# Optimization experiments

Hardware: AMD Instinct MI355X
Metric: run time of the kernel (lower is better)

Reference implementation:

```python
import jax, jax.numpy as jnp
import numpy as np

BN_EPS = 1e-5


def _gru(x, Wih, Whh, bih, bhh):
    # x: [B,S,D]; Wih: [3H,D]; Whh: [3H,H]; PyTorch gate order (r, z, n)
    B, S, D = x.shape
    H = Whh.shape[1]
    xg = jnp.einsum('bsd,gd->bsg', x, Wih) + bih  # [B,S,3H] precomputed input gates

    def step(h, xg_t):
        hg = h @ Whh.T + bhh
        xr, xz, xn = jnp.split(xg_t, 3, axis=-1)
        hr, hz, hn = jnp.split(hg, 3, axis=-1)
        r = jax.nn.sigmoid(xr + hr)
        z = jax.nn.sigmoid(xz + hz)
        n = jnp.tanh(xn + r * hn)
        h_new = (1.0 - z) * n + z * h
        return h_new, h_new

    h0 = jnp.zeros((B, H), x.dtype)
    _, hs = jax.lax.scan(step, h0, jnp.swapaxes(xg, 0, 1))  # [S,B,H]
    return jnp.swapaxes(hs, 0, 1)


def _lstm(x, Wih, Whh, bih, bhh):
    # x: [B,S,D]; PyTorch gate order (i, f, g, o)
    B, S, D = x.shape
    H = Whh.shape[1]
    xg = jnp.einsum('bsd,gd->bsg', x, Wih) + bih  # [B,S,4H]

    def step(carry, xg_t):
        h, c = carry
        g = xg_t + h @ Whh.T + bhh
        i, f, gg, o = jnp.split(g, 4, axis=-1)
        i = jax.nn.sigmoid(i)
        f = jax.nn.sigmoid(f)
        gg = jnp.tanh(gg)
        o = jax.nn.sigmoid(o)
        c_new = f * c + i * gg
        h_new = o * jnp.tanh(c_new)
        return (h_new, c_new), h_new

    h0 = jnp.zeros((B, H), x.dtype)
    c0 = jnp.zeros((B, H), x.dtype)
    _, hs = jax.lax.scan(step, (h0, c0), jnp.swapaxes(xg, 0, 1))
    return jnp.swapaxes(hs, 0, 1)


def setup_inputs() -> dict:
    key = jax.random.key(0)
    B, S, D, H = 64, 512, 40, 512
    ks = jax.random.split(key, 16)
    s_in = 1.0 / np.sqrt(H)

    def u(k, shape):
        return jax.random.uniform(k, shape, jnp.float32, -s_in, s_in)

    inp = {
        'x': jax.random.normal(ks[0], (B, S, D), jnp.float32),
        # rec1: GRU
        'gru_Wih': u(ks[1], (3 * H, D)),
        'gru_Whh': u(ks[2], (3 * H, H)),
        'gru_bih': u(ks[3], (3 * H,)),
        'gru_bhh': u(ks[4], (3 * H,)),
        # rec2: LSTM over [x, ssr] -> input D+1
        'lstm_Wih': u(ks[5], (4 * H, D + 1)),
        'lstm_Whh': u(ks[6], (4 * H, H)),
        'lstm_bih': u(ks[7], (4 * H,)),
        'lstm_bhh': u(ks[8], (4 * H,)),
        # fc1/fc2/fc3: hidden -> 1
        'fc1_w': u(ks[9], (1, H)), 'fc1_b': u(ks[10], (1,)),
        'fc2_w': u(ks[11], (1, H)), 'fc2_b': u(ks[12], (1,)),
        'fc3_w': u(ks[13], (1, H)), 'fc3_b': u(ks[14], (1,)),
        # BatchNorm1d affine params
        'bn_gamma': jnp.ones((H,), jnp.float32),
        'bn_beta': jnp.zeros((H,), jnp.float32),
    }
    return inp


def reference(x, gru_Wih, gru_Whh, gru_bih, gru_bhh,
              lstm_Wih, lstm_Whh, lstm_bih, lstm_bhh,
              fc1_w, fc1_b, fc2_w, fc2_b, fc3_w, fc3_b,
              bn_gamma, bn_beta):
    B, S, D = x.shape
    o1 = _gru(x, gru_Wih, gru_Whh, gru_bih, gru_bhh)  # [B,S,H]
    # BatchNorm1d (training mode): per-channel stats over (batch, time)
    mean = jnp.mean(o1, axis=(0, 1))
    var = jnp.mean((o1 - mean) ** 2, axis=(0, 1))
    o1 = (o1 - mean) * jax.lax.rsqrt(var + BN_EPS) * bn_gamma + bn_beta
    # gated scalar channel (dropout p=0 is identity)
    sr = jax.nn.relu(o1 @ fc1_w.T + fc1_b)            # [B,S,1]
    w = jnp.abs(jax.nn.sigmoid(o1 @ fc2_w.T + fc2_b))  # [B,S,1]
    ssr = sr * (w + 1.0)                              # [B,S,1]
    x2 = jnp.concatenate([x, ssr], axis=2)            # [B,S,D+1]
    o2 = _lstm(x2, lstm_Wih, lstm_Whh, lstm_bih, lstm_bhh)
    out = jax.nn.relu(o2 @ fc3_w.T + fc3_b)           # [B,S,1]
    return out, ssr
```

## Files before the change

kernel.cpp:

```cpp
#include <hip/hip_runtime.h>
#include <stdint.h>

#define MB 16
#define GW 16
#define NU 32
#define HD 512
#define SEQ 512
#define DX 40

using short8 = __attribute__((ext_vector_type(8))) short;
using f32x4  = __attribute__((ext_vector_type(4))) float;

__device__ __forceinline__ unsigned short f2bf(float f) {
  uint32_t u = __builtin_bit_cast(uint32_t, f);
  u += 0x7fffu + ((u >> 16) & 1u);
  return (unsigned short)(u >> 16);
}
__device__ __forceinline__ float sigm(float x) { return 1.0f / (1.0f + __expf(-x)); }


__global__ __launch_bounds__(512, 2) void gru_kernel(
    const float* __restrict__ x, const float* __restrict__ Wih,
    const float* __restrict__ Whh, const float* __restrict__ bih,
    const float* __restrict__ bhh, unsigned* __restrict__ flags,
    unsigned short* __restrict__ hbuf, float* __restrict__ o1,
    float* __restrict__ stats)
{
  const int wg = blockIdx.x & (GW - 1);
  const int g  = blockIdx.x >> 4;
  const int tid = threadIdx.x;
  const int wave = tid >> 6;
  const int lane = tid & 63;
  const int u0 = wg * NU;
  const int bg = g * MB;

  __shared__ unsigned short h_s[MB][520];
  __shared__ unsigned short x_s[MB][72];
  __shared__ float gate_s[3][MB][NU];
  __shared__ float xn_s[MB][NU];

  for (int i = tid; i < MB * 32; i += 512) x_s[i >> 5][40 + (i & 31)] = 0;

  short8 bfrag[18];
  const int myGate = wave >> 1;
  const int ut = wave & 1;
  const int kq = (lane >> 4) * 8;
  if (wave < 6) {
    const int row = myGate * HD + u0 + ut * 16 + (lane & 15);
    for (int kt = 0; kt < 16; ++kt) {
      const float* p = Whh + (size_t)row * HD + kt * 32 + kq;
      short8 f;
#pragma unroll
      for (int j = 0; j < 8; ++j) f[j] = (short)f2bf(p[j]);
      bfrag[kt] = f;
    }
    for (int kt = 16; kt < 18; ++kt) {
      short8 f;
#pragma unroll
      for (int j = 0; j < 8; ++j) {
        int c = kt * 32 + kq + j - HD;
        float v = (myGate < 2 && c < DX) ? Wih[(size_t)row * DX + c] : 0.0f;
        f[j] = (short)f2bf(v);
      }
      bfrag[kt] = f;
    }
  } else {
    const int row = 2 * HD + u0 + (wave - 6) * 16 + (lane & 15);
    for (int kt = 0; kt < 2; ++kt) {
      short8 f;
#pragma unroll
      for (int j = 0; j < 8; ++j) {
        int c = kt * 32 + kq + j;
        f[j] = (short)((c < DX) ? f2bf(Wih[(size_t)row * DX + c]) : 0);
      }
      bfrag[kt] = f;
    }
  }

  const int sb = tid >> 5;
  const int su = tid & 31;
  float hprev = 0.0f, ssum = 0.0f, ssq = 0.0f;
  const float b_r  = bih[u0 + su] + bhh[u0 + su];
  const float b_z  = bih[HD + u0 + su] + bhh[HD + u0 + su];
  const float b_in = bih[2 * HD + u0 + su];
  const float b_hn = bhh[2 * HD + u0 + su];

  unsigned* gf = flags + g * GW * 16;
  unsigned* myProdFlag = gf + ((tid & 127) >> 3) * 16;

  for (int t = 0; t < SEQ; ++t) {
    const unsigned long long* hin64 =
        (const unsigned long long*)(hbuf + ((size_t)g * 2 + (t & 1)) * MB * HD);
    uint32_t* hout32 =
        (uint32_t*)(hbuf + ((size_t)g * 2 + ((t + 1) & 1)) * MB * HD);

    {
      while (__hip_atomic_load(myProdFlag, __ATOMIC_RELAXED,
                               __HIP_MEMORY_SCOPE_AGENT) < (unsigned)t)
        __builtin_amdgcn_s_sleep(1);
#pragma unroll
      for (int it = 0; it < 4; ++it) {
        int q = it * 512 + tid;
        unsigned long long v = __hip_atomic_load(hin64 + q, __ATOMIC_RELAXED,
                                                 __HIP_MEMORY_SCOPE_AGENT);
        *(unsigned long long*)(&h_s[q >> 7][(q & 127) * 4]) = v;
      }
    }
    {
      int b = tid >> 5, c = tid & 31;
      const float* xr = x + ((size_t)(bg + b) * SEQ + t) * DX;
      x_s[b][c] = f2bf(xr[c]);
      if (c < 8) x_s[b][32 + c] = f2bf(xr[32 + c]);
    }
    __syncthreads();

    if (wave < 6) {
      const int m = lane & 15;
      f32x4 acc = {0.f, 0.f, 0.f, 0.f};
#pragma unroll
      for (int kt = 0; kt < 16; ++kt) {
        short8 a = *(const short8*)(&h_s[m][kt * 32 + kq]);
        acc = __builtin_amdgcn_mfma_f32_16x16x32_bf16(a, bfrag[kt], acc, 0, 0, 0);
      }
      short8 ax0 = *(const short8*)(&x_s[m][kq]);
      short8 ax1 = *(const short8*)(&x_s[m][32 + kq]);
      acc = __builtin_amdgcn_mfma_f32_16x16x32_bf16(ax0, bfrag[16], acc, 0, 0, 0);
      acc = __builtin_amdgcn_mfma_f32_16x16x32_bf16(ax1, bfrag[17], acc, 0, 0, 0);
#pragma unroll
      for (int r = 0; r < 4; ++r)
        gate_s[myGate][(lane >> 4) * 4 + r][ut * 16 + (lane & 15)] = acc[r];
    } else {
      const int m = lane & 15;
      f32x4 acc = {0.f, 0.f, 0.f, 0.f};
      short8 ax0 = *(const short8*)(&x_s[m][kq]);
      short8 ax1 = *(const short8*)(&x_s[m][32 + kq]);
      acc = __builtin_amdgcn_mfma_f32_16x16x32_bf16(ax0, bfrag[0], acc, 0, 0, 0);
      acc = __builtin_amdgcn_mfma_f32_16x16x32_bf16(ax1, bfrag[1], acc, 0, 0, 0);
#pragma unroll
      for (int r = 0; r < 4; ++r)
        xn_s[(lane >> 4) * 4 + r][(wave - 6) * 16 + (lane & 15)] = acc[r];
    }
    __syncthreads();

    float r_ = sigm(gate_s[0][sb][su] + b_r);
    float z_ = sigm(gate_s[1][sb][su] + b_z);
    float n_ = tanhf(xn_s[sb][su] + b_in + r_ * (gate_s[2][sb][su] + b_hn));
    float h = (1.0f - z_) * n_ + z_ * hprev;
    hprev = h;
    ssum += h; ssq += h * h;
    {
      float hp = __shfl_xor(h, 1);
      if ((tid & 1) == 0) {
        uint32_t packed = (uint32_t)f2bf(h) | ((uint32_t)f2bf(hp) << 16);
        __hip_atomic_store(hout32 + ((sb * HD + u0 + su) >> 1), packed,
                           __ATOMIC_RELAXED, __HIP_MEMORY_SCOPE_AGENT);
      }
    }
    __syncthreads();

    if (tid == 0)
      __hip_atomic_store(gf + wg * 16, (unsigned)(t + 1), __ATOMIC_RELAXED,
                         __HIP_MEMORY_SCOPE_AGENT);
    o1[((size_t)(bg + sb) * SEQ + t) * HD + u0 + su] = h;
  }

  atomicAdd(&stats[u0 + su], ssum);
  atomicAdd(&stats[HD + u0 + su], ssq);
}

__global__ __launch_bounds__(512, 2) void lstm_kernel(
    const float* __restrict__ x, const float* __restrict__ Wih,
    const float* __restrict__ Whh, const float* __restrict__ bih,
    const float* __restrict__ bhh, const float* __restrict__ ssr,
    unsigned* __restrict__ flags, unsigned short* __restrict__ hbuf,
    float* __restrict__ o2)
{
  const int wg = blockIdx.x & (GW - 1);
  const int g  = blockIdx.x >> 4;
  const int tid = threadIdx.x;
  const int wave = tid >> 6;
  const int lane = tid & 63;
  const int u0 = wg * NU;
  const int bg = g * MB;

  __shared__ unsigned short h_s[MB][520];
  __shared__ unsigned short x_s[MB][72];
  __shared__ float gate_s[4][MB][NU];

  for (int i = tid; i < MB * 32; i += 512) x_s[i >> 5][40 + (i & 31)] = 0;

  short8 bfrag[18];
  const int myGate = wave >> 1;
  const int ut = wave & 1;
  const int kq = (lane >> 4) * 8;
  {
    const int row = myGate * HD + u0 + ut * 16 + (lane & 15);
    for (int kt = 0; kt < 16; ++kt) {
      const float* p = Whh + (size_t)row * HD + kt * 32 + kq;
      short8 f;
#pragma unroll
      for (int j = 0; j < 8; ++j) f[j] = (short)f2bf(p[j]);
      bfrag[kt] = f;
    }
    for (int kt = 16; kt < 18; ++kt) {
      short8 f;
#pragma unroll
      for (int j = 0; j < 8; ++j) {
        int c = kt * 32 + kq + j - HD;
        float v = (c < 41) ? Wih[(size_t)row * 41 + c] : 0.0f;
        f[j] = (short)f2bf(v);
      }
      bfrag[kt] = f;
    }
  }

  const int sb = tid >> 5;
  const int su = tid & 31;
  float creg = 0.0f;
  const float b_i = bih[u0 + su] + bhh[u0 + su];
  const float b_f = bih[HD + u0 + su] + bhh[HD + u0 + su];
  const float b_g = bih[2 * HD + u0 + su] + bhh[2 * HD + u0 + su];
  const float b_o = bih[3 * HD + u0 + su] + bhh[3 * HD + u0 + su];

  unsigned* gf = flags + g * GW * 16;
  unsigned* myProdFlag = gf + ((tid & 127) >> 3) * 16;

  for (int t = 0; t < SEQ; ++t) {
    const unsigned long long* hin64 =
        (const unsigned long long*)(hbuf + ((size_t)g * 2 + (t & 1)) * MB * HD);
    uint32_t* hout32 =
        (uint32_t*)(hbuf + ((size_t)g * 2 + ((t + 1) & 1)) * MB * HD);

    {
      while (__hip_atomic_load(myProdFlag, __ATOMIC_RELAXED,
                               __HIP_MEMORY_SCOPE_AGENT) < (unsigned)t)
        __builtin_amdgcn_s_sleep(1);
#pragma unroll
      for (int it = 0; it < 4; ++it) {
        int q = it * 512 + tid;
        unsigned long long v = __hip_atomic_load(hin64 + q, __ATOMIC_RELAXED,
                                                 __HIP_MEMORY_SCOPE_AGENT);
        *(unsigned long long*)(&h_s[q >> 7][(q & 127) * 4]) = v;
      }
    }
    {
      int b = tid >> 5, c = tid & 31;
      const float* xr = x + ((size_t)(bg + b) * SEQ + t) * DX;
      x_s[b][c] = f2bf(xr[c]);
      if (c < 8) x_s[b][32 + c] = f2bf(xr[32 + c]);
      if (c == 8) x_s[b][40] = f2bf(ssr[(size_t)(bg + b) * SEQ + t]);
    }
    __syncthreads();

    {
      const int m = lane & 15;
      f32x4 acc = {0.f, 0.f, 0.f, 0.f};
#pragma unroll
      for (int kt = 0; kt < 16; ++kt) {
        short8 a = *(const short8*)(&h_s[m][kt * 32 + kq]);
        acc = __builtin_amdgcn_mfma_f32_16x16x32_bf16(a, bfrag[kt], acc, 0, 0, 0);
      }
      short8 ax0 = *(const short8*)(&x_s[m][kq]);
      short8 ax1 = *(const short8*)(&x_s[m][32 + kq]);
      acc = __builtin_amdgcn_mfma_f32_16x16x32_bf16(ax0, bfrag[16], acc, 0, 0, 0);
      acc = __builtin_amdgcn_mfma_f32_16x16x32_bf16(ax1, bfrag[17], acc, 0, 0, 0);
#pragma unroll
      for (int r = 0; r < 4; ++r)
        gate_s[myGate][(lane >> 4) * 4 + r][ut * 16 + (lane & 15)] = acc[r];
    }
    __syncthreads();

    float gi = sigm(gate_s[0][sb][su] + b_i);
    float gf_ = sigm(gate_s[1][sb][su] + b_f);
    float gg = tanhf(gate_s[2][sb][su] + b_g);
    float go = sigm(gate_s[3][sb][su] + b_o);
    creg = gf_ * creg + gi * gg;
    float h = go * tanhf(creg);
    {
      float hp = __shfl_xor(h, 1);
      if ((tid & 1) == 0) {
        uint32_t packed = (uint32_t)f2bf(h) | ((uint32_t)f2bf(hp) << 16);
        __hip_atomic_store(hout32 + ((sb * HD + u0 + su) >> 1), packed,
                           __ATOMIC_RELAXED, __HIP_MEMORY_SCOPE_AGENT);
      }
    }
    __syncthreads();

    if (tid == 0)
      __hip_atomic_store(gf + wg * 16, (unsigned)(t + 1), __ATOMIC_RELAXED,
                         __HIP_MEMORY_SCOPE_AGENT);
    o2[((size_t)(bg + sb) * SEQ + t) * HD + u0 + su] = h;
  }
}

__global__ __launch_bounds__(512) void coef_kernel(
    const float* __restrict__ stats, const float* __restrict__ fc1_w,
    const float* __restrict__ fc1_b, const float* __restrict__ fc2_w,
    const float* __restrict__ fc2_b, const float* __restrict__ gamma,
    const float* __restrict__ beta, float* __restrict__ coef)
{
  __shared__ float r1[512], r2[512];
  const int j = threadIdx.x;
  const float inv_n = 1.0f / 32768.0f;
  float mean = stats[j] * inv_n;
  float var = stats[HD + j] * inv_n - mean * mean;
  float scale = gamma[j] * rsqrtf(var + 1e-5f);
  float shift = beta[j] - mean * scale;
  coef[j] = fc1_w[j] * scale;
  coef[HD + j] = fc2_w[j] * scale;
  r1[j] = fc1_w[j] * shift;
  r2[j] = fc2_w[j] * shift;
  __syncthreads();
  for (int s = 256; s > 0; s >>= 1) {
    if (j < s) { r1[j] += r1[j + s]; r2[j] += r2[j + s]; }
    __syncthreads();
  }
  if (j == 0) {
    coef[2 * HD] = r1[0] + fc1_b[0];
    coef[2 * HD + 1] = r2[0] + fc2_b[0];
  }
}

__global__ __launch_bounds__(256) void ssr_kernel(
    const float* __restrict__ o1, const float* __restrict__ coef,
    float* __restrict__ ssr_ws, float* __restrict__ dssr)
{
  const int row = blockIdx.x * 4 + (threadIdx.x >> 6);
  const int lane = threadIdx.x & 63;
  const float* p = o1 + (size_t)row * HD + lane * 8;
  float s1 = 0.f, s2 = 0.f;
#pragma unroll
  for (int j = 0; j < 8; ++j) {
    float v = p[j];
    s1 += v * coef[lane * 8 + j];
    s2 += v * coef[HD + lane * 8 + j];
  }
#pragma unroll
  for (int off = 32; off > 0; off >>= 1) {
    s1 += __shfl_down(s1, off);
    s2 += __shfl_down(s2, off);
  }
  if (lane == 0) {
    float sr = fmaxf(s1 + coef[2 * HD], 0.0f);
    float w = fabsf(sigm(s2 + coef[2 * HD + 1]));
    float v = sr * (1.0f + w);
    ssr_ws[row] = v;
    dssr[row] = v;
  }
}

__global__ __launch_bounds__(256) void out_kernel(
    const float* __restrict__ o2, const float* __restrict__ fc3_w,
    const float* __restrict__ fc3_b, float* __restrict__ dout)
{
  const int row = blockIdx.x * 4 + (threadIdx.x >> 6);
  const int lane = threadIdx.x & 63;
  const float* p = o2 + (size_t)row * HD + lane * 8;
  float s = 0.f;
#pragma unroll
  for (int j = 0; j < 8; ++j) s += p[j] * fc3_w[lane * 8 + j];
#pragma unroll
  for (int off = 32; off > 0; off >>= 1) s += __shfl_down(s, off);
  if (lane == 0) dout[row] = fmaxf(s + fc3_b[0], 0.0f);
}

extern "C" void kernel_launch(void* const* d_in, const int* in_sizes, int n_in,
                              void* d_out, int out_size, void* d_ws, size_t ws_size,
                              hipStream_t stream) {
  (void)in_sizes; (void)n_in; (void)out_size; (void)ws_size;
  const float* x    = (const float*)d_in[0];
  const float* gWih = (const float*)d_in[1];
  const float* gWhh = (const float*)d_in[2];
  const float* gbih = (const float*)d_in[3];
  const float* gbhh = (const float*)d_in[4];
  const float* lWih = (const float*)d_in[5];
  const float* lWhh = (const float*)d_in[6];
  const float* lbih = (const float*)d_in[7];
  const float* lbhh = (const float*)d_in[8];
  const float* fc1w = (const float*)d_in[9];
  const float* fc1b = (const float*)d_in[10];
  const float* fc2w = (const float*)d_in[11];
  const float* fc2b = (const float*)d_in[12];
  const float* fc3w = (const float*)d_in[13];
  const float* fc3b = (const float*)d_in[14];
  const float* gam  = (const float*)d_in[15];
  const float* bet  = (const float*)d_in[16];
  float* out = (float*)d_out;

  char* ws = (char*)d_ws;
  unsigned* flags_g = (unsigned*)(ws + 0);
  unsigned* flags_l = (unsigned*)(ws + 4096);
  float* stats      = (float*)(ws + 8192);
  float* coef       = (float*)(ws + 16384);
  float* ssr_ws     = (float*)(ws + 32768);
  unsigned short* hbuf_g = (unsigned short*)(ws + 262144);
  unsigned short* hbuf_l = (unsigned short*)(ws + 393216);
  float* o1 = (float*)(ws + 1048576);
  float* o2 = o1 + (size_t)64 * SEQ * HD;

  hipMemsetAsync(ws, 0, 12288, stream);
  hipMemsetAsync(ws + 262144, 0, 262144, stream);

  gru_kernel<<<dim3(64), dim3(512), 0, stream>>>(x, gWih, gWhh, gbih, gbhh,
                                                 flags_g, hbuf_g, o1, stats);
  coef_kernel<<<dim3(1), dim3(512), 0, stream>>>(stats, fc1w, fc1b, fc2w, fc2b,
                                                 gam, bet, coef);
  ssr_kernel<<<dim3(8192), dim3(256), 0, stream>>>(o1, coef, ssr_ws, out + 32768);
  lstm_kernel<<<dim3(64), dim3(512), 0, stream>>>(x, lWih, lWhh, lbih, lbhh, ssr_ws,
                                                  flags_l, hbuf_l, o2);
  out_kernel<<<dim3(8192), dim3(256), 0, stream>>>(o2, fc3w, fc3b, out);
}
```

Measured before the change: 3.240 ms.

## Warp-specialize recurrent kernels with dedicated communication waves and LDS spin sync

Adds two communication waves per workgroup in both the GRU and LSTM kernels (640 threads). These waves publish the packed hidden state to global memory, raise the cross-block flag, and prefetch the next step's h and x into double-buffered LDS. The compute waves swap __syncthreads for counter-based LDS spin waits, and the elementwise threads now handle two batch rows each. Splitting the MFMA accumulation into two chains shortens the dependency latency. The aim is to take global communication and the full barriers off the per-step critical path, at the cost of more complex synchronisation and possible memory-ordering fragility.

Measured after the change: 3.542 ms. 1.09x slower.

```diff
diff --git a/kernel.cpp b/kernel.cpp
--- a/kernel.cpp
+++ b/kernel.cpp
@@ -1,15 +1,16 @@
 #include <hip/hip_runtime.h>
 #include <stdint.h>
 
-#define MB 16
 #define GW 16
 #define NU 32
 #define HD 512
 #define SEQ 512
 #define DX 40
+#define MB 16
 
 using short8 = __attribute__((ext_vector_type(8))) short;
 using f32x4  = __attribute__((ext_vector_type(4))) float;
+typedef unsigned long long u64;
 
 __device__ __forceinline__ unsigned short f2bf(float f) {
   uint32_t u = __builtin_bit_cast(uint32_t, f);
@@ -18,13 +19,14 @@
 }
 __device__ __forceinline__ float sigm(float x) { return 1.0f / (1.0f + __expf(-x)); }
 
-
-__global__ __launch_bounds__(512, 2) void gru_kernel(
+#define MFMA_B16(a, b, c) __builtin_amdgcn_mfma_f32_16x16x32_bf16((a), (b), (c), 0, 0, 0)
+
+
+__global__ __launch_bounds__(640, 1) void gru_kernel(
     const float* __restrict__ x, const float* __restrict__ Wih,
     const float* __restrict__ Whh, const float* __restrict__ bih,
     const float* __restrict__ bhh, unsigned* __restrict__ flags,
-    unsigned short* __restrict__ hbuf, float* __restrict__ o1,
-    float* __restrict__ stats)
+    u64* __restrict__ hbuf, float* __restrict__ o1, float* __restrict__ stats)
 {
   const int wg = blockIdx.x & (GW - 1);
   const int g  = blockIdx.x >> 4;
@@ -34,12 +36,12 @@
   const int u0 = wg * NU;
   const int bg = g * MB;
 
-  __shared__ unsigned short h_s[MB][520];
-  __shared__ unsigned short x_s[MB][72];
+  __shared__ __align__(16) unsigned short h_s[2][MB][520];
+  __shared__ __align__(16) unsigned short x_s[2][MB][72];
   __shared__ float gate_s[3][MB][NU];
   __shared__ float xn_s[MB][NU];
-
-  for (int i = tid; i < MB * 32; i += 512) x_s[i >> 5][40 + (i & 31)] = 0;
+  __shared__ uint32_t h_stage[256];
+  __shared__ uint32_t sync_s[4];
 
   short8 bfrag[18];
   const int myGate = wave >> 1;
@@ -64,7 +66,7 @@
       }
       bfrag[kt] = f;
     }
-  } else {
+  } else if (wave < 8) {
     const int row = 2 * HD + u0 + (wave - 6) * 16 + (lane & 15);
     for (int kt = 0; kt < 2; ++kt) {
       short8 f;
@@ -79,100 +81,166 @@
 
   const int sb = tid >> 5;
   const int su = tid & 31;
-  float hprev = 0.0f, ssum = 0.0f, ssq = 0.0f;
-  const float b_r  = bih[u0 + su] + bhh[u0 + su];
-  const float b_z  = bih[HD + u0 + su] + bhh[HD + u0 + su];
-  const float b_in = bih[2 * HD + u0 + su];
-  const float b_hn = bhh[2 * HD + u0 + su];
+  float b_r = 0.f, b_z = 0.f, b_in = 0.f, b_hn = 0.f;
+  if (tid < 256) {
+    b_r  = bih[u0 + su] + bhh[u0 + su];
+    b_z  = bih[HD + u0 + su] + bhh[HD + u0 + su];
+    b_in = bih[2 * HD + u0 + su];
+    b_hn = bhh[2 * HD + u0 + su];
+  }
+
+  for (int i = tid; i < 4160; i += 640) ((u64*)h_s)[i] = 0ull;
+  for (int i = tid; i < 576;  i += 640) ((u64*)x_s)[i] = 0ull;
+  if (tid < 4) sync_s[tid] = 0;
+  __syncthreads();
+  {
+    int r = tid / 40, c = tid % 40;
+    x_s[0][r][c] = f2bf(x[((size_t)(bg + r) * SEQ) * DX + c]);
+  }
+  __syncthreads();
 
   unsigned* gf = flags + g * GW * 16;
-  unsigned* myProdFlag = gf + ((tid & 127) >> 3) * 16;
-
-  for (int t = 0; t < SEQ; ++t) {
-    const unsigned long long* hin64 =
-        (const unsigned long long*)(hbuf + ((size_t)g * 2 + (t & 1)) * MB * HD);
-    uint32_t* hout32 =
-        (uint32_t*)(hbuf + ((size_t)g * 2 + ((t + 1) & 1)) * MB * HD);
-
-    {
-      while (__hip_atomic_load(myProdFlag, __ATOMIC_RELAXED,
-                               __HIP_MEMORY_SCOPE_AGENT) < (unsigned)t)
+
+  if (wave < 8) {
+    float hpA = 0.f, hpB = 0.f, ssum = 0.f, ssq = 0.f;
+    for (int t = 0; t < SEQ; ++t) {
+      if (t) {
+        while (__hip_atomic_load(&sync_s[2], __ATOMIC_ACQUIRE,
+                                 __HIP_MEMORY_SCOPE_WORKGROUP) < 2u * (unsigned)t)
+          __builtin_amdgcn_s_sleep(1);
+      }
+      const int p = t & 1;
+      if (wave < 6) {
+        const int m = lane & 15;
+        f32x4 a0 = {0.f, 0.f, 0.f, 0.f}, a1 = {0.f, 0.f, 0.f, 0.f};
+#pragma unroll
+        for (int kt = 0; kt < 16; kt += 2) {
+          short8 ha0 = *(const short8*)(&h_s[p][m][kt * 32 + kq]);
+          short8 ha1 = *(const short8*)(&h_s[p][m][(kt + 1) * 32 + kq]);
+          a0 = MFMA_B16(ha0, bfrag[kt], a0);
+          a1 = MFMA_B16(ha1, bfrag[kt + 1], a1);
+        }
+        short8 ax0 = *(const short8*)(&x_s[p][m][kq]);
+        short8 ax1 = *(const short8*)(&x_s[p][m][32 + kq]);
+        a0 = MFMA_B16(ax0, bfrag[16], a0);
+        a1 = MFMA_B16(ax1, bfrag[17], a1);
+        f32x4 acc = a0 + a1;
+#pragma unroll
+        for (int r = 0; r < 4; ++r)
+          gate_s[myGate][(lane >> 4) * 4 + r][ut * 16 + (lane & 15)] = acc[r];
+      } else {
+        const int m = lane & 15;
+        f32x4 acc = {0.f, 0.f, 0.f, 0.f};
+        short8 ax0 = *(const short8*)(&x_s[p][m][kq]);
+        short8 ax1 = *(const short8*)(&x_s[p][m][32 + kq]);
+        acc = MFMA_B16(ax0, bfrag[0], acc);
+        acc = MFMA_B16(ax1, bfrag[1], acc);
+#pragma unroll
+        for (int r = 0; r < 4; ++r)
+          xn_s[(lane >> 4) * 4 + r][(wave - 6) * 16 + (lane & 15)] = acc[r];
+      }
+      asm volatile("s_waitcnt lgkmcnt(0)" ::: "memory");
+      if (lane == 0)
+        __hip_atomic_fetch_add(&sync_s[0], 1u, __ATOMIC_RELAXED,
+                               __HIP_MEMORY_SCOPE_WORKGROUP);
+      if (tid < 256) {
+        while (__hip_atomic_load(&sync_s[0], __ATOMIC_ACQUIRE,
+                                 __HIP_MEMORY_SCOPE_WORKGROUP) < 8u * (unsigned)(t + 1))
+          __builtin_amdgcn_s_sleep(1);
+        float rA = sigm(gate_s[0][sb][su] + b_r);
+        float zA = sigm(gate_s[1][sb][su] + b_z);
+        float nA = tanhf(xn_s[sb][su] + b_in + rA * (gate_s[2][sb][su] + b_hn));
+        float hA = (1.0f - zA) * nA + zA * hpA;
+        float rB = sigm(gate_s[0][sb + 8][su] + b_r);
+        float zB = sigm(gate_s[1][sb + 8][su] + b_z);
+        float nB = tanhf(xn_s[sb + 8][su] + b_in + rB * (gate_s[2][sb + 8][su] + b_hn));
+        float hB = (1.0f - zB) * nB + zB * hpB;
+        hpA = hA; hpB = hB;
+        ssum += hA + hB; ssq += hA * hA + hB * hB;
+        o1[((size_t)(bg + sb) * SEQ + t) * HD + u0 + su] = hA;
+        o1[((size_t)(bg + sb + 8) * SEQ + t) * HD + u0 + su] = hB;
+        float pA = __shfl_xor(hA, 1);
+        float pB = __shfl_xor(hB, 1);
+        if ((su & 1) == 0) {
+          h_stage[sb * 16 + (su >> 1)] =
+              (uint32_t)f2bf(hA) | ((uint32_t)f2bf(pA) << 16);
+          h_stage[(sb + 8) * 16 + (su >> 1)] =
+              (uint32_t)f2bf(hB) | ((uint32_t)f2bf(pB) << 16);
+        }
+        asm volatile("s_waitcnt lgkmcnt(0)" ::: "memory");
+        if (lane == 0)
+          __hip_atomic_fetch_add(&sync_s[1], 1u, __ATOMIC_RELAXED,
+                                 __HIP_MEMORY_SCOPE_WORKGROUP);
+      }
+    }
+    if (tid < 256) {
+      atomicAdd(&stats[u0 + su], ssum);
+      atomicAdd(&stats[HD + u0 + su], ssq);
+    }
+  } else {
+    const int ct = tid - 512;
+    const int prow = ct >> 3;
+    const int pquad = ct & 7;
+    unsigned* myFlag = gf + prow * 16;
+    for (int u = 0; u < SEQ - 1; ++u) {
+      while (__hip_atomic_load(&sync_s[1], __ATOMIC_ACQUIRE,
+                               __HIP_MEMORY_SCOPE_WORKGROUP) < 4u * (unsigned)(u + 1))
         __builtin_amdgcn_s_sleep(1);
-#pragma unroll
-      for (int it = 0; it < 4; ++it) {
-        int q = it * 512 + tid;
-        unsigned long long v = __hip_atomic_load(hin64 + q, __ATOMIC_RELAXED,
-                                                 __HIP_MEMORY_SCOPE_AGENT);
-        *(unsigned long long*)(&h_s[q >> 7][(q & 127) * 4]) = v;
-      }
-    }
-    {
-      int b = tid >> 5, c = tid & 31;
-      const float* xr = x + ((size_t)(bg + b) * SEQ + t) * DX;
-      x_s[b][c] = f2bf(xr[c]);
-      if (c < 8) x_s[b][32 + c] = f2bf(xr[32 + c]);
-    }
-    __syncthreads();
-
-    if (wave < 6) {
-      const int m = lane & 15;
-      f32x4 acc = {0.f, 0.f, 0.f, 0.f};
-#pragma unroll
-      for (int kt = 0; kt < 16; ++kt) {
-        short8 a = *(const short8*)(&h_s[m][kt * 32 + kq]);
-        acc = __builtin_amdgcn_mfma_f32_16x16x32_bf16(a, bfrag[kt], acc, 0, 0, 0);
-      }
-      short8 ax0 = *(const short8*)(&x_s[m][kq]);
-      short8 ax1 = *(const short8*)(&x_s[m][32 + kq]);
-      acc = __builtin_amdgcn_mfma_f32_16x16x32_bf16(ax0, bfrag[16], acc, 0, 0, 0);
-      acc = __builtin_amdgcn_mfma_f32_16x16x32_bf16(ax1, bfrag[17], acc, 0, 0, 0);
-#pragma unroll
-      for (int r = 0; r < 4; ++r)
-        gate_s[myGate][(lane >> 4) * 4 + r][ut * 16 + (lane & 15)] = acc[r];
-    } else {
-      const int m = lane & 15;
-      f32x4 acc = {0.f, 0.f, 0.f, 0.f};
-      short8 ax0 = *(const short8*)(&x_s[m][kq]);
-      short8 ax1 = *(const short8*)(&x_s[m][32 + kq]);
-      acc = __builtin_amdgcn_mfma_f32_16x16x32_bf16(ax0, bfrag[0], acc, 0, 0, 0);
-      acc = __builtin_amdgcn_mfma_f32_16x16x32_bf16(ax1, bfrag[1], acc, 0, 0, 0);
-#pragma unroll
-      for (int r = 0; r < 4; ++r)
-        xn_s[(lane >> 4) * 4 + r][(wave - 6) * 16 + (lane & 15)] = acc[r];
-    }
-    __syncthreads();
-
-    float r_ = sigm(gate_s[0][sb][su] + b_r);
-    float z_ = sigm(gate_s[1][sb][su] + b_z);
-    float n_ = tanhf(xn_s[sb][su] + b_in + r_ * (gate_s[2][sb][su] + b_hn));
-    float h = (1.0f - z_) * n_ + z_ * hprev;
-    hprev = h;
-    ssum += h; ssq += h * h;
-    {
-      float hp = __shfl_xor(h, 1);
-      if ((tid & 1) == 0) {
-        uint32_t packed = (uint32_t)f2bf(h) | ((uint32_t)f2bf(hp) << 16);
-        __hip_atomic_store(hout32 + ((sb * HD + u0 + su) >> 1), packed,
-                           __ATOMIC_RELAXED, __HIP_MEMORY_SCOPE_AGENT);
-      }
-    }
-    __syncthreads();
-
-    if (tid == 0)
-      __hip_atomic_store(gf + wg * 16, (unsigned)(t + 1), __ATOMIC_RELAXED,
-                         __HIP_MEMORY_SCOPE_AGENT);
-    o1[((size_t)(bg + sb) * SEQ + t) * HD + u0 + su] = h;
-  }
-
-  atomicAdd(&stats[u0 + su], ssum);
-  atomicAdd(&stats[HD + u0 + su], ssq);
-}
-
-__global__ __launch_bounds__(512, 2) void lstm_kernel(
+      uint32_t w0 = h_stage[prow * 16 + pquad * 2];
+      uint32_t w1 = h_stage[prow * 16 + pquad * 2 + 1];
+      u64 pub = ((u64)w1 << 32) | (u64)w0;
+      u64* hb = hbuf + ((size_t)g * 2 + ((u + 1) & 1)) * 2048;
+      __hip_atomic_store(hb + prow * 128 + wg * 8 + pquad, pub,
+                         __ATOMIC_RELAXED, __HIP_MEMORY_SCOPE_AGENT);
+      asm volatile("s_waitcnt vmcnt(0)" ::: "memory");
+      if (lane == 0)
+        __hip_atomic_fetch_add(&sync_s[3], 1u, __ATOMIC_RELAXED,
+                               __HIP_MEMORY_SCOPE_WORKGROUP);
+      if (wave == 8) {
+        while (__hip_atomic_load(&sync_s[3], __ATOMIC_ACQUIRE,
+                                 __HIP_MEMORY_SCOPE_WORKGROUP) < 2u * (unsigned)(u + 1))
+          __builtin_amdgcn_s_sleep(1);
+        if (lane == 0)
+          __hip_atomic_store(gf + wg * 16, (unsigned)(u + 1),
+                             __ATOMIC_RELAXED, __HIP_MEMORY_SCOPE_AGENT);
+      }
+      float xv[5];
+      const int xi = ct * 5;
+#pragma unroll
+      for (int i = 0; i < 5; ++i) {
+        int idx = xi + i, r = idx / 40, c = idx % 40;
+        xv[i] = x[((size_t)(bg + r) * SEQ + (u + 1)) * DX + c];
+      }
+      while (__hip_atomic_load(myFlag, __ATOMIC_RELAXED,
+                               __HIP_MEMORY_SCOPE_AGENT) < (unsigned)(u + 1))
+        __builtin_amdgcn_s_sleep(1);
+      u64 hv[16];
+#pragma unroll
+      for (int i = 0; i < 16; ++i)
+        hv[i] = __hip_atomic_load(hb + i * 128 + ct, __ATOMIC_RELAXED,
+                                  __HIP_MEMORY_SCOPE_AGENT);
+      const int np = (u + 1) & 1;
+#pragma unroll
+      for (int i = 0; i < 16; ++i)
+        *(u64*)(&h_s[np][i][ct * 4]) = hv[i];
+#pragma unroll
+      for (int i = 0; i < 5; ++i) {
+        int idx = xi + i, r = idx / 40, c = idx % 40;
+        x_s[np][r][c] = f2bf(xv[i]);
+      }
+      asm volatile("s_waitcnt lgkmcnt(0)" ::: "memory");
+      if (lane == 0)
+        __hip_atomic_fetch_add(&sync_s[2], 1u, __ATOMIC_RELAXED,
+                               __HIP_MEMORY_SCOPE_WORKGROUP);
+    }
+  }
+}
+
+__global__ __launch_bounds__(640, 1) void lstm_kernel(
     const float* __restrict__ x, const float* __restrict__ Wih,
     const float* __restrict__ Whh, const float* __restrict__ bih,
     const float* __restrict__ bhh, const float* __restrict__ ssr,
-    unsigned* __restrict__ flags, unsigned short* __restrict__ hbuf,
+    unsigned* __restrict__ flags, u64* __restrict__ hbuf,
     float* __restrict__ o2)
 {
   const int wg = blockIdx.x & (GW - 1);
@@ -183,17 +251,17 @@
   const int u0 = wg * NU;
   const int bg = g * MB;
 
-  __shared__ unsigned short h_s[MB][520];
-  __shared__ unsigned short x_s[MB][72];
+  __shared__ __align__(16) unsigned short h_s[2][MB][520];
+  __shared__ __align__(16) unsigned short x_s[2][MB][72];
   __shared__ float gate_s[4][MB][NU];
-
-  for (int i = tid; i < MB * 32; i += 512) x_s[i >> 5][40 + (i & 31)] = 0;
+  __shared__ uint32_t h_stage[256];
+  __shared__ uint32_t sync_s[4];
 
   short8 bfrag[18];
   const int myGate = wave >> 1;
   const int ut = wave & 1;
   const int kq = (lane >> 4) * 8;
-  {
+  if (wave < 8) {
     const int row = myGate * HD + u0 + ut * 16 + (lane & 15);
     for (int kt = 0; kt < 16; ++kt) {
       const float* p = Whh + (size_t)row * HD + kt * 32 + kq;
@@ -216,80 +284,150 @@
 
   const int sb = tid >> 5;
   const int su = tid & 31;
-  float creg = 0.0f;
-  const float b_i = bih[u0 + su] + bhh[u0 + su];
-  const float b_f = bih[HD + u0 + su] + bhh[HD + u0 + su];
-  const float b_g = bih[2 * HD + u0 + su] + bhh[2 * HD + u0 + su];
-  const float b_o = bih[3 * HD + u0 + su] + bhh[3 * HD + u0 + su];
+  float b_i = 0.f, b_f = 0.f, b_g = 0.f, b_o = 0.f;
+  if (tid < 256) {
+    b_i = bih[u0 + su] + bhh[u0 + su];
+    b_f = bih[HD + u0 + su] + bhh[HD + u0 + su];
+    b_g = bih[2 * HD + u0 + su] + bhh[2 * HD + u0 + su];
+    b_o = bih[3 * HD + u0 + su] + bhh[3 * HD + u0 + su];
+  }
+
+  for (int i = tid; i < 4160; i += 640) ((u64*)h_s)[i] = 0ull;
+  for (int i = tid; i < 576;  i += 640) ((u64*)x_s)[i] = 0ull;
+  if (tid < 4) sync_s[tid] = 0;
+  __syncthreads();
+  {
+    int r = tid / 40, c = tid % 40;
+    x_s[0][r][c] = f2bf(x[((size_t)(bg + r) * SEQ) * DX + c]);
+  }
+  if (tid < 16) x_s[0][tid][40] = f2bf(ssr[(size_t)(bg + tid) * SEQ]);
+  __syncthreads();
 
   unsigned* gf = flags + g * GW * 16;
-  unsigned* myProdFlag = gf + ((tid & 127) >> 3) * 16;
-
-  for (int t = 0; t < SEQ; ++t) {
-    const unsigned long long* hin64 =
-        (const unsigned long long*)(hbuf + ((size_t)g * 2 + (t & 1)) * MB * HD);
-    uint32_t* hout32 =
-        (uint32_t*)(hbuf + ((size_t)g * 2 + ((t + 1) & 1)) * MB * HD);
-
-    {
-      while (__hip_atomic_load(myProdFlag, __ATOMIC_RELAXED,
-                               __HIP_MEMORY_SCOPE_AGENT) < (unsigned)t)
+
+  if (wave < 8) {
+    float cA = 0.f, cB = 0.f;
+    for (int t = 0; t < SEQ; ++t) {
+      if (t) {
+        while (__hip_atomic_load(&sync_s[2], __ATOMIC_ACQUIRE,
+                                 __HIP_MEMORY_SCOPE_WORKGROUP) < 2u * (unsigned)t)
+          __builtin_amdgcn_s_sleep(1);
+      }
+      const int p = t & 1;
+      {
+        const int m = lane & 15;
+        f32x4 a0 = {0.f, 0.f, 0.f, 0.f}, a1 = {0.f, 0.f, 0.f, 0.f};
+#pragma unroll
+        for (int kt = 0; kt < 16; kt += 2) {
+          short8 ha0 = *(const short8*)(&h_s[p][m][kt * 32 + kq]);
+          short8 ha1 = *(const short8*)(&h_s[p][m][(kt + 1) * 32 + kq]);
+          a0 = MFMA_B16(ha0, bfrag[kt], a0);
+          a1 = MFMA_B16(ha1, bfrag[kt + 1], a1);
+        }
+        short8 ax0 = *(const short8*)(&x_s[p][m][kq]);
+        short8 ax1 = *(const short8*)(&x_s[p][m][32 + kq]);
+        a0 = MFMA_B16(ax0, bfrag[16], a0);
+        a1 = MFMA_B16(ax1, bfrag[17], a1);
+        f32x4 acc = a0 + a1;
+#pragma unroll
+        for (int r = 0; r < 4; ++r)
+          gate_s[myGate][(lane >> 4) * 4 + r][ut * 16 + (lane & 15)] = acc[r];
+      }
+      asm volatile("s_waitcnt lgkmcnt(0)" ::: "memory");
+      if (lane == 0)
+        __hip_atomic_fetch_add(&sync_s[0], 1u, __ATOMIC_RELAXED,
+                               __HIP_MEMORY_SCOPE_WORKGROUP);
+      if (tid < 256) {
+        while (__hip_atomic_load(&sync_s[0], __ATOMIC_ACQUIRE,
+                                 __HIP_MEMORY_SCOPE_WORKGROUP) < 8u * (unsigned)(t + 1))
+          __builtin_amdgcn_s_sleep(1);
+        float giA = sigm(gate_s[0][sb][su] + b_i);
+        float gfA = sigm(gate_s[1][sb][su] + b_f);
+        float ggA = tanhf(gate_s[2][sb][su] + b_g);
+        float goA = sigm(gate_s[3][sb][su] + b_o);
+        cA = gfA * cA + giA * ggA;
+        float hA = goA * tanhf(cA);
+        float giB = sigm(gate_s[0][sb + 8][su] + b_i);
+        float gfB = sigm(gate_s[1][sb + 8][su] + b_f);
+        float ggB = tanhf(gate_s[2][sb + 8][su] + b_g);
+        float goB = sigm(gate_s[3][sb + 8][su] + b_o);
+        cB = gfB * cB + giB * ggB;
+        float hB = goB * tanhf(cB);
+        o2[((size_t)(bg + sb) * SEQ + t) * HD + u0 + su] = hA;
+        o2[((size_t)(bg + sb + 8) * SEQ + t) * HD + u0 + su] = hB;
+        float pA = __shfl_xor(hA, 1);
+        float pB = __shfl_xor(hB, 1);
+        if ((su & 1) == 0) {
+          h_stage[sb * 16 + (su >> 1)] =
+              (uint32_t)f2bf(hA) | ((uint32_t)f2bf(pA) << 16);
+          h_stage[(sb + 8) * 16 + (su >> 1)] =
+              (uint32_t)f2bf(hB) | ((uint32_t)f2bf(pB) << 16);
+        }
+        asm volatile("s_waitcnt lgkmcnt(0)" ::: "memory");
+        if (lane == 0)
+          __hip_atomic_fetch_add(&sync_s[1], 1u, __ATOMIC_RELAXED,
+                                 __HIP_MEMORY_SCOPE_WORKGROUP);
+      }
+    }
+  } else {
+    const int ct = tid - 512;
+    const int prow = ct >> 3;
+    const int pquad = ct & 7;
+    unsigned* myFlag = gf + prow * 16;
+    for (int u = 0; u < SEQ - 1; ++u) {
+      while (__hip_atomic_load(&sync_s[1], __ATOMIC_ACQUIRE,
+                               __HIP_MEMORY_SCOPE_WORKGROUP) < 4u * (unsigned)(u + 1))
         __builtin_amdgcn_s_sleep(1);
-#pragma unroll
-      for (int it = 0; it < 4; ++it) {
-        int q = it * 512 + tid;
-        unsigned long long v = __hip_atomic_load(hin64 + q, __ATOMIC_RELAXED,
-                                                 __HIP_MEMORY_SCOPE_AGENT);
-        *(unsigned long long*)(&h_s[q >> 7][(q & 127) * 4]) = v;
-      }
-    }
-    {
-      int b = tid >> 5, c = tid & 31;
-      const float* xr = x + ((size_t)(bg + b) * SEQ + t) * DX;
-      x_s[b][c] = f2bf(xr[c]);
-      if (c < 8) x_s[b][32 + c] = f2bf(xr[32 + c]);
-      if (c == 8) x_s[b][40] = f2bf(ssr[(size_t)(bg + b) * SEQ + t]);
-    }
-    __syncthreads();
-
-    {
-      const int m = lane & 15;
-      f32x4 acc = {0.f, 0.f, 0.f, 0.f};
-#pragma unroll
-      for (int kt = 0; kt < 16; ++kt) {
-        short8 a = *(const short8*)(&h_s[m][kt * 32 + kq]);
-        acc = __builtin_amdgcn_mfma_f32_16x16x32_bf16(a, bfrag[kt], acc, 0, 0, 0);
-      }
-      short8 ax0 = *(const short8*)(&x_s[m][kq]);
-      short8 ax1 = *(const short8*)(&x_s[m][32 + kq]);
-      acc = __builtin_amdgcn_mfma_f32_16x16x32_bf16(ax0, bfrag[16], acc, 0, 0, 0);
-      acc = __builtin_amdgcn_mfma_f32_16x16x32_bf16(ax1, bfrag[17], acc, 0, 0, 0);
-#pragma unroll
-      for (int r = 0; r < 4; ++r)
-        gate_s[myGate][(lane >> 4) * 4 + r][ut * 16 + (lane & 15)] = acc[r];
-    }
-    __syncthreads();
-
-    float gi = sigm(gate_s[0][sb][su] + b_i);
-    float gf_ = sigm(gate_s[1][sb][su] + b_f);
-    float gg = tanhf(gate_s[2][sb][su] + b_g);
-    float go = sigm(gate_s[3][sb][su] + b_o);
-    creg = gf_ * creg + gi * gg;
-    float h = go * tanhf(creg);
-    {
-      float hp = __shfl_xor(h, 1);
-      if ((tid & 1) == 0) {
-        uint32_t packed = (uint32_t)f2bf(h) | ((uint32_t)f2bf(hp) << 16);
-        __hip_atomic_store(hout32 + ((sb * HD + u0 + su) >> 1), packed,
-                           __ATOMIC_RELAXED, __HIP_MEMORY_SCOPE_AGENT);
-      }
-    }
-    __syncthreads();
-
-    if (tid == 0)
-      __hip_atomic_store(gf + wg * 16, (unsigned)(t + 1), __ATOMIC_RELAXED,
-                         __HIP_MEMORY_SCOPE_AGENT);
-    o2[((size_t)(bg + sb) * SEQ + t) * HD + u0 + su] = h;
+      uint32_t w0 = h_stage[prow * 16 + pquad * 2];
+      uint32_t w1 = h_stage[prow * 16 + pquad * 2 + 1];
+      u64 pub = ((u64)w1 << 32) | (u64)w0;
+      u64* hb = hbuf + ((size_t)g * 2 + ((u + 1) & 1)) * 2048;
+      __hip_atomic_store(hb + prow * 128 + wg * 8 + pquad, pub,
+                         __ATOMIC_RELAXED, __HIP_MEMORY_SCOPE_AGENT);
+      asm volatile("s_waitcnt vmcnt(0)" ::: "memory");
+      if (lane == 0)
+        __hip_atomic_fetch_add(&sync_s[3], 1u, __ATOMIC_RELAXED,
+                               __HIP_MEMORY_SCOPE_WORKGROUP);
+      if (wave == 8) {
+        while (__hip_atomic_load(&sync_s[3], __ATOMIC_ACQUIRE,
+                                 __HIP_MEMORY_SCOPE_WORKGROUP) < 2u * (unsigned)(u + 1))
+          __builtin_amdgcn_s_sleep(1);
+        if (lane == 0)
+          __hip_atomic_store(gf + wg * 16, (unsigned)(u + 1),
+                             __ATOMIC_RELAXED, __HIP_MEMORY_SCOPE_AGENT);
+      }
+      float xv[5];
+      const int xi = ct * 5;
+#pragma unroll
+      for (int i = 0; i < 5; ++i) {
+        int idx = xi + i, r = idx / 40, c = idx % 40;
+        xv[i] = x[((size_t)(bg + r) * SEQ + (u + 1)) * DX + c];
+      }
+      float sv = 0.f;
+      if (ct < 16) sv = ssr[(size_t)(bg + ct) * SEQ + (u + 1)];
+      while (__hip_atomic_load(myFlag, __ATOMIC_RELAXED,
+                               __HIP_MEMORY_SCOPE_AGENT) < (unsigned)(u + 1))
+        __builtin_amdgcn_s_sleep(1);
+      u64 hv[16];
+#pragma unroll
+      for (int i = 0; i < 16; ++i)
+        hv[i] = __hip_atomic_load(hb + i * 128 + ct, __ATOMIC_RELAXED,
+                                  __HIP_MEMORY_SCOPE_AGENT);
+      const int np = (u + 1) & 1;
+#pragma unroll
+      for (int i = 0; i < 16; ++i)
+        *(u64*)(&h_s[np][i][ct * 4]) = hv[i];
+#pragma unroll
+      for (int i = 0; i < 5; ++i) {
+        int idx = xi + i, r = idx / 40, c = idx % 40;
+        x_s[np][r][c] = f2bf(xv[i]);
+      }
+      if (ct < 16) x_s[np][ct][40] = f2bf(sv);
+      asm volatile("s_waitcnt lgkmcnt(0)" ::: "memory");
+      if (lane == 0)
+        __hip_atomic_fetch_add(&sync_s[2], 1u, __ATOMIC_RELAXED,
+                               __HIP_MEMORY_SCOPE_WORKGROUP);
+    }
   }
 }
 
@@ -390,23 +528,22 @@
   char* ws = (char*)d_ws;
   unsigned* flags_g = (unsigned*)(ws + 0);
   unsigned* flags_l = (unsigned*)(ws + 4096);
-  float* stats      = (float*)(ws + 8192);
-  float* coef       = (float*)(ws + 16384);
+  float* stats      = (float*)(ws + 16384);
+  float* coef       = (float*)(ws + 24576);
   float* ssr_ws     = (float*)(ws + 32768);
-  unsigned short* hbuf_g = (unsigned short*)(ws + 262144);
-  unsigned short* hbuf_l = (unsigned short*)(ws + 393216);
+  u64* hbuf_g       = (u64*)(ws + 262144);
+  u64* hbuf_l       = (u64*)(ws + 393216);
   float* o1 = (float*)(ws + 1048576);
   float* o2 = o1 + (size_t)64 * SEQ * HD;
 
-  hipMemsetAsync(ws, 0, 12288, stream);
-  hipMemsetAsync(ws + 262144, 0, 262144, stream);
-
-  gru_kernel<<<dim3(64), dim3(512), 0, stream>>>(x, gWih, gWhh, gbih, gbhh,
+  hipMemsetAsync(ws, 0, 20480, stream);
+
+  gru_kernel<<<dim3(64), dim3(640), 0, stream>>>(x, gWih, gWhh, gbih, gbhh,
                                                  flags_g, hbuf_g, o1, stats);
   coef_kernel<<<dim3(1), dim3(512), 0, stream>>>(stats, fc1w, fc1b, fc2w, fc2b,
                                                  gam, bet, coef);
   ssr_kernel<<<dim3(8192), dim3(256), 0, stream>>>(o1, coef, ssr_ws, out + 32768);
-  lstm_kernel<<<dim3(64), dim3(512), 0, stream>>>(x, lWih, lWhh, lbih, lbhh, ssr_ws,
+  lstm_kernel<<<dim3(64), dim3(640), 0, stream>>>(x, lWih, lWhh, lbih, lbhh, ssr_ws,
                                                   flags_l, hbuf_l, o2);
   out_kernel<<<dim3(8192), dim3(256), 0, stream>>>(o2, fc3w, fc3b, out);
 }
```
